# Kernel tuning notes

Hardware: AMD Instinct MI355X
Metric: run time of the kernel (lower is better)

Reference implementation:

```python
import jax, jax.numpy as jnp
import numpy as np

NUM_QUBITS = 10
NUM_LAYERS = 5
OBS = 10          # observation_size == num_qubits (required by input_scaling indexing)
NUM_OUTPUTS = 4   # num_actions, discretize=False
BATCH = 4096


def _bcast(theta, n):
    # theta: scalar or (B,) -> broadcastable against (B, 2, 2, ..., 2)
    return jnp.reshape(jnp.asarray(theta), (-1,) + (1,) * n)


def _ry(st, theta, q, n):
    # st: (B,) + (2,)*n complex64; per-sample RY(theta) on qubit q
    t = _bcast(theta, n) * 0.5
    c, s = jnp.cos(t), jnp.sin(t)
    s0 = jax.lax.index_in_dim(st, 0, axis=q + 1, keepdims=True)
    s1 = jax.lax.index_in_dim(st, 1, axis=q + 1, keepdims=True)
    return jnp.concatenate([c * s0 - s * s1, s * s0 + c * s1], axis=q + 1)


def _rz(st, theta, q, n):
    t = _bcast(theta, n) * 0.5
    s0 = jax.lax.index_in_dim(st, 0, axis=q + 1, keepdims=True)
    s1 = jax.lax.index_in_dim(st, 1, axis=q + 1, keepdims=True)
    return jnp.concatenate([jnp.exp(-1j * t) * s0, jnp.exp(1j * t) * s1], axis=q + 1)


def _cnot(st, c, t):
    # flip target axis on the control=1 slab; pure index ops (no residuals in bwd)
    s0 = jax.lax.index_in_dim(st, 0, axis=c + 1, keepdims=True)
    s1 = jax.lax.index_in_dim(st, 1, axis=c + 1, keepdims=True)
    s1 = jnp.flip(s1, axis=t + 1)
    return jnp.concatenate([s0, s1], axis=c + 1)


def _layer(st, x, isc, w, n, obs):
    # isc: (2n,) input_scaling row, w: (2n,) weights row
    for i in range(obs):
        st = _ry(st, isc[i] * x[:, i], i, n)
        st = _rz(st, isc[i + obs] * x[:, i], i, n)
    for i in range(n):
        st = _rz(st, w[i], i, n)
    for i in range(n):
        st = _ry(st, w[i + n], i, n)
    if n == 2:
        st = _cnot(st, 0, 1)
    else:
        for i in range(n):
            st = _cnot(st, i, (i + 1) % n)
    return st


_layer_ckpt = jax.checkpoint(_layer, static_argnums=(4, 5))


def _circuit(x, input_scaling, weights, n, num_layers, obs, num_outputs):
    B = x.shape[0]
    st = jnp.zeros((B,) + (2,) * n, dtype=jnp.complex64)
    st = st.at[(slice(None),) + (0,) * n].set(1.0)  # |0...0>
    for layer in range(num_layers):
        st = _layer_ckpt(st, x, input_scaling[layer], weights[layer], n, obs)
    probs = jnp.real(st * jnp.conj(st))
    outs = []
    for i in range(num_outputs):
        axes = tuple(a for a in range(1, n + 1) if a != i + 1)
        pi = jnp.sum(probs, axis=axes)  # (B, 2)
        outs.append(pi[:, 0] - pi[:, 1])  # <Z_i>
    return jnp.stack(outs, axis=1)


def setup_inputs() -> dict:
    key = jax.random.key(0)
    k1, k2 = jax.random.split(key)
    x = jax.random.normal(k1, (BATCH, OBS), dtype=jnp.float32)
    input_scaling = jnp.ones((NUM_LAYERS, 2 * NUM_QUBITS), dtype=jnp.float32)
    weights = jax.random.uniform(k2, (NUM_LAYERS, 2 * NUM_QUBITS), minval=-np.pi, maxval=np.pi, dtype=jnp.float32)
    output_scaling = jnp.ones((NUM_OUTPUTS,), dtype=jnp.float32)
    return {"x": x, "input_scaling": input_scaling, "weights": weights, "output_scaling": output_scaling}


def reference(x, input_scaling, weights, output_scaling):
    z = _circuit(x, input_scaling, weights, NUM_QUBITS, NUM_LAYERS, OBS, NUM_OUTPUTS)
    return z * output_scaling  # (B, num_actions); discretize=False -> actions = scaled expvals
```

## Files before the change

### kernel.cpp

```cpp
#include <hip/hip_runtime.h>


constexpr int NQ  = 10;
constexpr int NL  = 5;
constexpr int OBS = 10;

typedef float f2 __attribute__((ext_vector_type(2)));

__device__ __forceinline__ float readlane_f(float v, int l) {
    return __int_as_float(__builtin_amdgcn_readlane(__float_as_int(v), l));
}
__device__ __forceinline__ float bperm_f(int byte_addr, float v) {
    return __int_as_float(__builtin_amdgcn_ds_bpermute(byte_addr, __float_as_int(v)));
}
template <int CTRL>
__device__ __forceinline__ float dpp_f(float v) {
    return __int_as_float(__builtin_amdgcn_update_dpp(
        0, __float_as_int(v), CTRL, 0xF, 0xF, true));
}
__device__ __forceinline__ float xor_lane(float v, int M, int a16, int a32) {
    switch (M) {
    case 1:  return dpp_f<0xB1>(v);
    case 2:  return dpp_f<0x4E>(v);
    case 8:  return dpp_f<0x128>(v);
    case 4:  return dpp_f<0x141>(dpp_f<0x1B>(v));
    case 16: return bperm_f(a16, v);
    default: return bperm_f(a32, v);
    }
}

template <int Q>
__device__ __forceinline__ void apply_gate(f2* c, int lane,
                                           float ur, float ui,
                                           float vr, float vi,
                                           int a16, int a32) {
    const f2 kUU  = {ur, ur};
    const f2 kUIm = {-ui, ui};
    const f2 kVVn = {-vr, -vr};
    const f2 kVV  = {vr, vr};
    const f2 kVIm = {-vi, vi};
    const f2 kUIp = {ui, -ui};
    if constexpr (Q < 4) {
        constexpr int m = 1 << (3 - Q);
#pragma unroll
        for (int r0 = 0; r0 < 16; ++r0) {
            if (r0 & m) continue;
            const int r1 = r0 | m;
            const f2 c0 = c[r0], c1 = c[r1];
            const f2 c0s = c0.yx, c1s = c1.yx;
            c[r0] = kUU*c0 + kUIm*c0s + kVVn*c1 + kVIm*c1s;
            c[r1] = kVV*c0 + kVIm*c0s + kUU*c1  + kUIp*c1s;
        }
    } else {
        constexpr int M = 1 << (9 - Q);
        const bool bit = (lane & M) != 0;
        const float Pi = bit ? -ui : ui;
        const float Qr = bit ?  vr : -vr;
        const f2 kUUb = {ur, ur};
        const f2 kPI  = {-Pi, Pi};
        const f2 kQR  = {Qr, Qr};
        const f2 kVIb = {-vi, vi};
#pragma unroll
        for (int r = 0; r < 16; ++r) {
            const f2 mv = c[r];
            f2 pv;
            pv.x = xor_lane(mv.x, M, a16, a32);
            pv.y = xor_lane(mv.y, M, a16, a32);
            c[r] = kUUb*mv + kPI*mv.yx + kQR*pv + kVIb*pv.yx;
        }
    }
}

__global__ __launch_bounds__(256, 4) void qsim_kernel(
    const float* __restrict__ x,
    const float* __restrict__ isc,
    const float* __restrict__ w,
    const float* __restrict__ oscale,
    float* __restrict__ out,
    int B)
{
    const int lane = threadIdx.x & 63;
    const int wid  = (blockIdx.x * blockDim.x + threadIdx.x) >> 6;
    if (wid >= B) return;

    float cUR, cUI, cVR, cVI;
    {
        const int g   = (lane < 50) ? lane : 49;
        const int q   = g % 10;
        const int lyr = g / 10;
        const float xq    = x[wid * OBS + q];
        const float alpha = isc[lyr * 2 * NQ + q]      * xq;
        const float beta  = isc[lyr * 2 * NQ + NQ + q] * xq;
        const float gamma = w[lyr * 2 * NQ + q];
        const float delta = w[lyr * 2 * NQ + NQ + q];
        float sa, ca, sp, cp, sd, cd;
        __sincosf(0.5f * alpha,          &sa, &ca);
        __sincosf(0.5f * (beta + gamma), &sp, &cp);
        __sincosf(0.5f * delta,          &sd, &cd);
        const float A = cd * ca, Bt = sd * sa;
        const float C = cd * sa, D  = sd * ca;
        cUR = (A - Bt) * cp;
        cUI = -(A + Bt) * sp;
        cVR = (C + D) * cp;
        cVI = (C - D) * sp;
    }

    const int a16 = (lane ^ 16) * 4;
    const int a32 = (lane ^ 32) * 4;
    const int cnot_src  = (lane ^ (lane >> 1));
    const int addr_even = cnot_src * 4;
    const int addr_odd  = (cnot_src ^ 32) * 4;

    const bool rev = (wid & 1) != 0;

    f2 c[16];

    {
        float Lr = 1.f, Li = 0.f;
#pragma unroll
        for (int q = 4; q < 10; ++q) {
            const float ur = readlane_f(cUR, q), ui = readlane_f(cUI, q);
            const float vr = readlane_f(cVR, q), vi = readlane_f(cVI, q);
            const int M = 1 << (9 - q);
            const float fr = (lane & M) ? vr : ur;
            const float fi = (lane & M) ? vi : ui;
            const float nr = Lr * fr - Li * fi;
            const float ni = Lr * fi + Li * fr;
            Lr = nr; Li = ni;
        }
        c[0] = (f2){Lr, Li};
#pragma unroll
        for (int r = 1; r < 16; ++r) c[r] = (f2){0.f, 0.f};
#pragma unroll
        for (int q = 3; q >= 0; --q) {
            const int m = 1 << (3 - q);
            const float ur = readlane_f(cUR, q), ui = readlane_f(cUI, q);
            const float vr = readlane_f(cVR, q), vi = readlane_f(cVI, q);
#pragma unroll
            for (int r0 = 0; r0 < 16; ++r0) {
                if (r0 >= m) continue;
                const f2 s = c[r0];
                c[r0 | m] = (f2){ s.x*vr - s.y*vi, s.x*vi + s.y*vr };
                c[r0]     = (f2){ s.x*ur - s.y*ui, s.x*ui + s.y*ur };
            }
        }
    }

#define SWAPR(i, j) { f2 _t = c[i]; c[i] = c[j]; c[j] = _t; }
#define G(Q) { const float ur = readlane_f(cUR, base + Q);                 \
               const float ui = readlane_f(cUI, base + Q);                 \
               const float vr = readlane_f(cVR, base + Q);                 \
               const float vi = readlane_f(cVI, base + Q);                 \
               apply_gate<Q>(c, lane, ur, ui, vr, vi, a16, a32); }

    for (int layer = 0; layer < NL; ++layer) {
        const int base = layer * NQ;

        if (layer > 0) {
            if (!rev) {
                G(0) G(1) G(2) G(3) G(4) G(5) G(6) G(7) G(8) G(9)
            } else {
                G(9) G(8) G(7) G(6) G(5) G(4) G(3) G(2) G(1) G(0)
            }
        }

        if (layer < NL - 1) {
            SWAPR(8, 12) SWAPR(9, 13) SWAPR(10, 14) SWAPR(11, 15)
            SWAPR(4, 6)  SWAPR(5, 7)  SWAPR(12, 14) SWAPR(13, 15)
            SWAPR(2, 3)  SWAPR(6, 7)  SWAPR(10, 11) SWAPR(14, 15)
#pragma unroll
            for (int r = 0; r < 16; ++r) {
                const int addr = (r & 1) ? addr_odd : addr_even;
                c[r].x = bperm_f(addr, c[r].x);
                c[r].y = bperm_f(addr, c[r].y);
            }
            const bool ctl = (lane & 1) != 0;
#pragma unroll
            for (int r = 0; r < 8; ++r) {
                const f2 t0 = c[r], t1 = c[r + 8];
                c[r]     = ctl ? t1 : t0;
                c[r + 8] = ctl ? t0 : t1;
            }
        }
    }

    const float sL = (__popc(lane) & 1) ? -1.f : 1.f;
    float z0 = 0.f, z1 = 0.f, z2 = 0.f, z3 = 0.f;
#pragma unroll
    for (int r = 0; r < 16; ++r) {
        const float pv  = c[r].x * c[r].x + c[r].y * c[r].y;
        const float pvl = sL * pv;
        z0 += (__popc(r & 7)  & 1) ? -pvl : pvl;
        z1 += (__popc(r & 12) & 1) ? -pv  : pv;
        z2 += (__popc(r & 14) & 1) ? -pv  : pv;
        z3 += (__popc(r & 15) & 1) ? -pv  : pv;
    }
#pragma unroll
    for (int m = 1; m < 64; m <<= 1) {
        z0 += xor_lane(z0, m, a16, a32);
        z1 += xor_lane(z1, m, a16, a32);
        z2 += xor_lane(z2, m, a16, a32);
        z3 += xor_lane(z3, m, a16, a32);
    }
    if (lane == 0) {
        out[wid * 4 + 0] = z0 * oscale[0];
        out[wid * 4 + 1] = z1 * oscale[1];
        out[wid * 4 + 2] = z2 * oscale[2];
        out[wid * 4 + 3] = z3 * oscale[3];
    }
#undef SWAPR
#undef G
}

extern "C" void kernel_launch(void* const* d_in, const int* in_sizes, int n_in,
                              void* d_out, int out_size, void* d_ws, size_t ws_size,
                              hipStream_t stream) {
    const float* x      = (const float*)d_in[0];
    const float* isc    = (const float*)d_in[1];
    const float* w      = (const float*)d_in[2];
    const float* oscale = (const float*)d_in[3];
    float* out = (float*)d_out;

    const int B = in_sizes[0] / OBS;
    const int threads = 256;
    const int blocks = (B * 64 + threads - 1) / threads;
    qsim_kernel<<<blocks, threads, 0, stream>>>(x, isc, w, oscale, out, B);
}
```

Measured before the change: 90.91 us.

## Fold CNOT ring permutation into gate coefficients and lane shuffles

Removes the per-layer ds_bpermute CNOT permutation in middle layers by folding the CNOT chain's basis relabeling into subsequent single-qubit gates: register swaps are interleaved between register gates and lane-controlled gates pick per-lane coefficients based on a control bit. Only the first layer boundary still uses the bpermute shuffle, and the final layer is specialized. Also drops the alternate gate ordering for odd waves. This trades cross-lane permute traffic for extra per-lane selects and coefficient setup, with risk of correctness subtleties in the folded basis mapping.

```diff
diff --git a/kernel.cpp b/kernel.cpp
--- a/kernel.cpp
+++ b/kernel.cpp
@@ -30,43 +30,65 @@
 }
 
 template <int Q>
-__device__ __forceinline__ void apply_gate(f2* c, int lane,
-                                           float ur, float ui,
-                                           float vr, float vi,
-                                           int a16, int a32) {
+__device__ __forceinline__ void reg_gate(f2* c, float ur, float ui,
+                                         float vr, float vi) {
     const f2 kUU  = {ur, ur};
     const f2 kUIm = {-ui, ui};
     const f2 kVVn = {-vr, -vr};
     const f2 kVV  = {vr, vr};
     const f2 kVIm = {-vi, vi};
     const f2 kUIp = {ui, -ui};
-    if constexpr (Q < 4) {
-        constexpr int m = 1 << (3 - Q);
-#pragma unroll
-        for (int r0 = 0; r0 < 16; ++r0) {
-            if (r0 & m) continue;
-            const int r1 = r0 | m;
-            const f2 c0 = c[r0], c1 = c[r1];
-            const f2 c0s = c0.yx, c1s = c1.yx;
-            c[r0] = kUU*c0 + kUIm*c0s + kVVn*c1 + kVIm*c1s;
-            c[r1] = kVV*c0 + kVIm*c0s + kUU*c1  + kUIp*c1s;
-        }
-    } else {
-        constexpr int M = 1 << (9 - Q);
-        const bool bit = (lane & M) != 0;
-        const float Pi = bit ? -ui : ui;
-        const float Qr = bit ?  vr : -vr;
-        const f2 kUUb = {ur, ur};
-        const f2 kPI  = {-Pi, Pi};
-        const f2 kQR  = {Qr, Qr};
-        const f2 kVIb = {-vi, vi};
+    constexpr int m = 1 << (3 - Q);
+#pragma unroll
+    for (int r0 = 0; r0 < 16; ++r0) {
+        if (r0 & m) continue;
+        const int r1 = r0 | m;
+        const f2 c0 = c[r0], c1 = c[r1];
+        const f2 c0s = c0.yx, c1s = c1.yx;
+        c[r0] = kUU*c0 + kUIm*c0s + kVVn*c1 + kVIm*c1s;
+        c[r1] = kVV*c0 + kVIm*c0s + kUU*c1  + kUIp*c1s;
+    }
+}
+
+template <int MT, int BQMASK, bool REGFOLD>
+__device__ __forceinline__ void lane_gate(f2* c, int lane,
+                                          float ur, float ui,
+                                          float vr, float vi,
+                                          int a16, int a32) {
+    const bool bt = (lane & MT) != 0;
+    if constexpr (REGFOLD) {
+        const float Pr0 = ur,              Pi0 = bt ? -ui : ui;
+        const float Qr0 = bt ? vr : -vr,   Qi0 = vi;
+        const float Pr1 = bt ? -vr : vr,   Pi1 = vi;
+        const float Qr1 = ur,              Qi1 = bt ? ui : -ui;
+        const f2 kP0 = {Pr0, Pr0}, kPs0 = {-Pi0, Pi0};
+        const f2 kQ0 = {Qr0, Qr0}, kQs0 = {-Qi0, Qi0};
+        const f2 kP1 = {Pr1, Pr1}, kPs1 = {-Pi1, Pi1};
+        const f2 kQ1 = {Qr1, Qr1}, kQs1 = {-Qi1, Qi1};
 #pragma unroll
         for (int r = 0; r < 16; ++r) {
             const f2 mv = c[r];
             f2 pv;
-            pv.x = xor_lane(mv.x, M, a16, a32);
-            pv.y = xor_lane(mv.y, M, a16, a32);
-            c[r] = kUUb*mv + kPI*mv.yx + kQR*pv + kVIb*pv.yx;
+            pv.x = xor_lane(mv.x, MT, a16, a32);
+            pv.y = xor_lane(mv.y, MT, a16, a32);
+            if (r & 1) c[r] = kP1*mv + kPs1*mv.yx + kQ1*pv + kQs1*pv.yx;
+            else       c[r] = kP0*mv + kPs0*mv.yx + kQ0*pv + kQs0*pv.yx;
+        }
+    } else {
+        const bool bq = (BQMASK != 0) && ((lane & BQMASK) != 0);
+        const float Pr = bq ? (bt ? -vr : vr) : ur;
+        const float Pi = bq ? vi : (bt ? -ui : ui);
+        const float Qr = bq ? ur : (bt ? vr : -vr);
+        const float Qi = bq ? (bt ? ui : -ui) : vi;
+        const f2 kP = {Pr, Pr}, kPs = {-Pi, Pi};
+        const f2 kQ = {Qr, Qr}, kQs = {-Qi, Qi};
+#pragma unroll
+        for (int r = 0; r < 16; ++r) {
+            const f2 mv = c[r];
+            f2 pv;
+            pv.x = xor_lane(mv.x, MT, a16, a32);
+            pv.y = xor_lane(mv.y, MT, a16, a32);
+            c[r] = kP*mv + kPs*mv.yx + kQ*pv + kQs*pv.yx;
         }
     }
 }
@@ -111,8 +133,6 @@
     const int addr_even = cnot_src * 4;
     const int addr_odd  = (cnot_src ^ 32) * 4;
 
-    const bool rev = (wid & 1) != 0;
-
     f2 c[16];
 
     {
@@ -147,41 +167,52 @@
     }
 
 #define SWAPR(i, j) { f2 _t = c[i]; c[i] = c[j]; c[j] = _t; }
-#define G(Q) { const float ur = readlane_f(cUR, base + Q);                 \
-               const float ui = readlane_f(cUI, base + Q);                 \
-               const float vr = readlane_f(cVR, base + Q);                 \
-               const float vi = readlane_f(cVI, base + Q);                 \
-               apply_gate<Q>(c, lane, ur, ui, vr, vi, a16, a32); }
-
-    for (int layer = 0; layer < NL; ++layer) {
+#define SW01 SWAPR(8, 12) SWAPR(9, 13) SWAPR(10, 14) SWAPR(11, 15)
+#define SW12 SWAPR(4, 6)  SWAPR(5, 7)  SWAPR(12, 14) SWAPR(13, 15)
+#define SW23 SWAPR(2, 3)  SWAPR(6, 7)  SWAPR(10, 11) SWAPR(14, 15)
+#define CONDSWAP90 { const bool ctl = (lane & 1) != 0;                        \
+    _Pragma("unroll")                                                         \
+    for (int r = 0; r < 8; ++r) {                                             \
+        const f2 t0 = c[r], t1 = c[r + 8];                                    \
+        c[r]     = ctl ? t1 : t0;                                             \
+        c[r + 8] = ctl ? t0 : t1;                                             \
+    } }
+#define COEFF(Q) const float ur = readlane_f(cUR, base + (Q));                \
+                 const float ui = readlane_f(cUI, base + (Q));                \
+                 const float vr = readlane_f(cVR, base + (Q));                \
+                 const float vi = readlane_f(cVI, base + (Q));
+#define RG(Q)            { COEFF(Q) reg_gate<Q>(c, ur, ui, vr, vi); }
+#define LG(Q, BQM, RF)   { COEFF(Q) lane_gate<(1 << (9 - (Q))), BQM, RF>(     \
+                               c, lane, ur, ui, vr, vi, a16, a32); }
+
+    {
+        SW01 SW12 SW23
+#pragma unroll
+        for (int r = 0; r < 16; ++r) {
+            const int addr = (r & 1) ? addr_odd : addr_even;
+            c[r].x = bperm_f(addr, c[r].x);
+            c[r].y = bperm_f(addr, c[r].y);
+        }
+        CONDSWAP90
+    }
+
+    for (int layer = 1; layer < NL - 1; ++layer) {
         const int base = layer * NQ;
-
-        if (layer > 0) {
-            if (!rev) {
-                G(0) G(1) G(2) G(3) G(4) G(5) G(6) G(7) G(8) G(9)
-            } else {
-                G(9) G(8) G(7) G(6) G(5) G(4) G(3) G(2) G(1) G(0)
-            }
-        }
-
-        if (layer < NL - 1) {
-            SWAPR(8, 12) SWAPR(9, 13) SWAPR(10, 14) SWAPR(11, 15)
-            SWAPR(4, 6)  SWAPR(5, 7)  SWAPR(12, 14) SWAPR(13, 15)
-            SWAPR(2, 3)  SWAPR(6, 7)  SWAPR(10, 11) SWAPR(14, 15)
-#pragma unroll
-            for (int r = 0; r < 16; ++r) {
-                const int addr = (r & 1) ? addr_odd : addr_even;
-                c[r].x = bperm_f(addr, c[r].x);
-                c[r].y = bperm_f(addr, c[r].y);
-            }
-            const bool ctl = (lane & 1) != 0;
-#pragma unroll
-            for (int r = 0; r < 8; ++r) {
-                const f2 t0 = c[r], t1 = c[r + 8];
-                c[r]     = ctl ? t1 : t0;
-                c[r + 8] = ctl ? t0 : t1;
-            }
-        }
+        RG(0) RG(1) SW01 RG(2) SW12 RG(3) SW23
+        LG(4, 0, true)
+        LG(5, 32, false)
+        LG(6, 16, false)
+        LG(7, 8,  false)
+        LG(8, 4,  false)
+        LG(9, 2,  false)
+        CONDSWAP90
+    }
+
+    {
+        const int base = 4 * NQ;
+        RG(0) RG(1) RG(2) RG(3)
+        LG(4, 0, false) LG(5, 0, false) LG(6, 0, false)
+        LG(7, 0, false) LG(8, 0, false) LG(9, 0, false)
     }
 
     const float sL = (__popc(lane) & 1) ? -1.f : 1.f;
@@ -209,7 +240,13 @@
         out[wid * 4 + 3] = z3 * oscale[3];
     }
 #undef SWAPR
-#undef G
+#undef SW01
+#undef SW12
+#undef SW23
+#undef CONDSWAP90
+#undef COEFF
+#undef RG
+#undef LG
 }
 
 extern "C" void kernel_launch(void* const* d_in, const int* in_sizes, int n_in,
```

Result: no change. 92.22 us (+1.4%).
